# Kernel tuning notes

Hardware: AMD Instinct MI355X
Metric: run time of the kernel (lower is better)

## Reference

```python
import jax, jax.numpy as jnp
import numpy as np

# pywt 'db4' decomposition filters (8 taps)
DEC_LO = jnp.array([-0.010597401784997278, 0.032883011666982945, 0.030841381835986965,
                    -0.18703481171888114, -0.02798376941698385, 0.6308807679295904,
                    0.7148465705525415, 0.23037781330885523], dtype=jnp.float32)
DEC_HI = jnp.array([-0.23037781330885523, 0.7148465705525415, -0.6308807679295904,
                    -0.02798376941698385, 0.18703481171888114, 0.030841381835986965,
                    -0.032883011666982945, -0.010597401784997278], dtype=jnp.float32)
LEVELS = 3


def _dwt_step(sig, lo, hi):
    """One pywt dwt level, mode='symmetric'. sig: [M, S] -> (cA, cD) each [M, (S+F-1)//2]."""
    F = lo.shape[0]
    # symmetric extension by F-1 on each side; drop first sample so stride-2
    # correlation picks the odd-indexed valid-convolution outputs (pywt convention)
    ext = jnp.pad(sig, ((0, 0), (F - 1, F - 1)), mode='symmetric')[:, 1:]
    # true convolution = correlation with flipped filters
    kern = jnp.stack([lo[::-1], hi[::-1]])[:, None, :]          # [2, 1, F]
    y = jax.lax.conv_general_dilated(ext[:, None, :], kern, (2,), 'VALID')  # [M, 2, out]
    return y[:, 0], y[:, 1]


def _resize(c, T):
    """Match torch: truncate if longer than T, else F.interpolate linear align_corners=False."""
    S = c.shape[-1]
    if S == T:
        return c
    if S > T:
        return c[..., :T]
    pos = (jnp.arange(T, dtype=c.dtype) + 0.5) * (S / T) - 0.5
    pos = jnp.clip(pos, 0.0, S - 1)
    lo = jnp.floor(pos).astype(jnp.int32)
    hi = jnp.minimum(lo + 1, S - 1)
    w = pos - lo.astype(c.dtype)
    return c[..., lo] * (1.0 - w) + c[..., hi] * w


def setup_inputs() -> dict:
    key = jax.random.key(0)
    x = jax.random.normal(key, (16, 2048, 512, 1), dtype=jnp.float32)
    return {"x": x}


def reference(x):
    B, T, N, _ = x.shape
    sig = x[:, :, :, 0].transpose(0, 2, 1).reshape(B * N, T)  # [B*N, T]
    a = sig
    details = []
    for _ in range(LEVELS):
        a, d = _dwt_step(a, DEC_LO, DEC_HI)
        details.append(d)
    coeffs = [a] + details[::-1]  # pywt order: [cA_L, cD_L, ..., cD_1]
    out = jnp.stack([_resize(c, T) for c in coeffs], axis=-1)  # [B*N, T, L+1]
    return out.reshape(B, N, T, LEVELS + 1)
```

## Files before the change

### kernel.cpp

```cpp
#include <hip/hip_runtime.h>


#define TPB   256
#define ROWS  4
#define TLEN  2048
#define NCH   512
#define RSTRIDE 3080
#define CA3_OFF 0
#define CD3_OFF 520
#define CD2_OFF 1027
#define CD1_OFF 2048

typedef float f32x4 __attribute__((ext_vector_type(4)));

__constant__ float LO[8] = {-0.010597401784997278f,  0.032883011666982945f,  0.030841381835986965f,
                            -0.18703481171888114f,  -0.02798376941698385f,   0.6308807679295904f,
                             0.7148465705525415f,    0.23037781330885523f};
__constant__ float HI[8] = {-0.23037781330885523f,   0.7148465705525415f,   -0.6308807679295904f,
                            -0.02798376941698385f,   0.18703481171888114f,   0.030841381835986965f,
                            -0.032883011666982945f, -0.010597401784997278f};
__constant__ float RLO[8] = { 0.23037781330885523f,   0.7148465705525415f,   0.6308807679295904f,
                             -0.02798376941698385f,  -0.18703481171888114f,  0.030841381835986965f,
                              0.032883011666982945f, -0.010597401784997278f};
__constant__ float RHI[8] = {-0.010597401784997278f, -0.032883011666982945f, 0.030841381835986965f,
                              0.18703481171888114f,  -0.02798376941698385f,  -0.6308807679295904f,
                              0.7148465705525415f,   -0.23037781330885523f};

__device__ __forceinline__ int sym_idx(int e, int S) {
    int m = e - 6;
    m = (m < 0) ? (-1 - m) : m;
    m = (m >= S) ? (2 * S - 1 - m) : m;
    return m;
}

__device__ __forceinline__ void dwt_level_wave(float* rowp, int in_off, int S,
                                               int lo_off, int hi_off, int lane) {
    const int O    = (S + 7) >> 1;
    const int jmax = (S - 2) >> 1;
    for (int j = lane; j < O; j += 64) {
        float slo = 0.0f, shi = 0.0f;
        if (j >= 3 && j <= jmax) {
            const float* p = rowp + in_off + 2 * j - 6;
            float v[8];
            *(float2*)&v[0] = ((const float2*)p)[0];
            *(float2*)&v[2] = ((const float2*)p)[1];
            *(float2*)&v[4] = ((const float2*)p)[2];
            *(float2*)&v[6] = ((const float2*)p)[3];
            #pragma unroll
            for (int k = 0; k < 8; ++k) {
                slo = fmaf(RLO[k], v[k], slo);
                shi = fmaf(RHI[k], v[k], shi);
            }
        } else {
            const float* in = rowp + in_off;
            const int e0 = 2 * j + 7;
            #pragma unroll
            for (int k = 0; k < 8; ++k) {
                const float v = in[sym_idx(e0 - k, S)];
                slo = fmaf(LO[k], v, slo);
                shi = fmaf(HI[k], v, shi);
            }
        }
        rowp[lo_off + j] = slo;
        rowp[hi_off + j] = shi;
    }
}

__device__ __forceinline__ void lerp_coef(int S, int t, int& i0, int& i1, float& w) {
    const float scale = (float)S * (1.0f / 2048.0f);
    float p = ((float)t + 0.5f) * scale - 0.5f;
    p = fminf(fmaxf(p, 0.0f), (float)(S - 1));
    i0 = (int)p;
    i1 = min(i0 + 1, S - 1);
    w = p - (float)i0;
}

__device__ __forceinline__ float mix2(float a, float b, float w) {
    return a * (1.0f - w) + b * w;
}

__global__ __launch_bounds__(TPB)
void dwt_kernel(const float* __restrict__ x, float* __restrict__ out) {
    __shared__ float lds[ROWS * RSTRIDE];
    const int tid = threadIdx.x;

    const int nwg   = gridDim.x;
    const int chunk = nwg >> 3;
    const int p     = blockIdx.x;
    const int bid   = (p & 7) * chunk + (p >> 3);

    const int row0 = bid * ROWS;
    const int b    = row0 >> 9;
    const int n0   = row0 & 511;

    const float4* src = (const float4*)(x + (size_t)b * TLEN * NCH + n0);
    #pragma unroll
    for (int i = 0; i < TLEN / TPB; ++i) {
        const int t = tid + i * TPB;
        const float4 v = src[t * (NCH / 4)];
        lds[0 * RSTRIDE + t] = v.x;
        lds[1 * RSTRIDE + t] = v.y;
        lds[2 * RSTRIDE + t] = v.z;
        lds[3 * RSTRIDE + t] = v.w;
    }
    __syncthreads();

    const int wave = tid >> 6;
    const int lane = tid & 63;
    float* rowp = lds + wave * RSTRIDE;

    dwt_level_wave(rowp, 0, 2048, 0, CD1_OFF, lane);
    dwt_level_wave(rowp, 0, 1027, 0, CD2_OFF, lane);
    dwt_level_wave(rowp, 0,  517, 0, CD3_OFF, lane);

    f32x4* dst = (f32x4*)out + (size_t)(row0 + wave) * TLEN;
    #pragma unroll 4
    for (int i = 0; i < TLEN / 64; ++i) {
        const int t = lane + i * 64;
        int i0a, i1a; float wa; lerp_coef( 262, t, i0a, i1a, wa);
        int i0b, i1b; float wb; lerp_coef( 517, t, i0b, i1b, wb);
        int i0c, i1c; float wc; lerp_coef(1027, t, i0c, i1c, wc);
        f32x4 o;
        o.x = mix2(rowp[CA3_OFF + i0a], rowp[CA3_OFF + i1a], wa);
        o.y = mix2(rowp[CD3_OFF + i0a], rowp[CD3_OFF + i1a], wa);
        o.z = mix2(rowp[CD2_OFF + i0b], rowp[CD2_OFF + i1b], wb);
        o.w = mix2(rowp[CD1_OFF + i0c], rowp[CD1_OFF + i1c], wc);
        __builtin_nontemporal_store(o, &dst[t]);
    }
}

extern "C" void kernel_launch(void* const* d_in, const int* in_sizes, int n_in,
                              void* d_out, int out_size, void* d_ws, size_t ws_size,
                              hipStream_t stream) {
    const float* x = (const float*)d_in[0];
    float* out = (float*)d_out;
    const int n_rows = 16 * 512;
    dim3 grid(n_rows / ROWS), block(TPB);
    hipLaunchKernelGGL(dwt_kernel, grid, block, 0, stream, x, out);
}
```

Baseline: 66.08 us.

## Warp-specialize into a persistent double-buffered load/compute/store pipeline

Replaces the one-tile-per-block kernel with a persistent kernel of 256 blocks, each processing 8 row tiles. Within a block, two waves load input into a double-buffered LDS area, four waves run the three DWT levels, and four waves do the interpolation and stores, all synchronized by per-stage barriers. The DWT level function also moves the symmetric-boundary outputs into a separate pre-pass so the main loop has no branch. The aim is to overlap global loads, compute and stores across tiles, at the cost of about 130KB of LDS, one block per CU and fewer waves issuing memory traffic.

```diff
diff --git a/kernel.cpp b/kernel.cpp
--- a/kernel.cpp
+++ b/kernel.cpp
@@ -1,15 +1,19 @@
 #include <hip/hip_runtime.h>
 
 
-#define TPB   256
-#define ROWS  4
-#define TLEN  2048
-#define NCH   512
-#define RSTRIDE 3080
-#define CA3_OFF 0
-#define CD3_OFF 520
-#define CD2_OFF 1027
-#define CD1_OFF 2048
+#define TPB      640
+#define NT       8
+#define ROWS     4
+#define TLEN     2048
+#define NCH      512
+#define IBSTRIDE 2056
+#define CSTRIDE  2088
+#define CD1o 0
+#define CD2o 1032
+#define CD3o 1552
+#define CA3o 1816
+#define IB_FLOATS  (2 * ROWS * IBSTRIDE)
+#define LDS_BYTES  ((IB_FLOATS + 2 * ROWS * CSTRIDE) * 4)
 
 typedef float f32x4 __attribute__((ext_vector_type(4)));
 
@@ -26,6 +30,11 @@
                               0.18703481171888114f,  -0.02798376941698385f,  -0.6308807679295904f,
                               0.7148465705525415f,   -0.23037781330885523f};
 
+__device__ __forceinline__ void bar_lgkm() {
+    asm volatile("s_waitcnt lgkmcnt(0)" ::: "memory");
+    __builtin_amdgcn_s_barrier();
+}
+
 __device__ __forceinline__ int sym_idx(int e, int S) {
     int m = e - 6;
     m = (m < 0) ? (-1 - m) : m;
@@ -33,37 +42,41 @@
     return m;
 }
 
-__device__ __forceinline__ void dwt_level_wave(float* rowp, int in_off, int S,
-                                               int lo_off, int hi_off, int lane) {
+__device__ __forceinline__ void wave_level(const float* in, int S,
+                                           float* lo, float* hi, int lane) {
     const int O    = (S + 7) >> 1;
     const int jmax = (S - 2) >> 1;
-    for (int j = lane; j < O; j += 64) {
+    const int NB   = O - (jmax - 2);
+
+    float blo = 0.0f, bhi = 0.0f;
+    int bj = 0;
+    if (lane < NB) {
+        bj = (lane < 3) ? lane : (jmax + lane - 2);
+        const int e0 = 2 * bj + 7;
+        #pragma unroll
+        for (int k = 0; k < 8; ++k) {
+            const float v = in[sym_idx(e0 - k, S)];
+            blo = fmaf(LO[k], v, blo);
+            bhi = fmaf(HI[k], v, bhi);
+        }
+    }
+    for (int j = 3 + lane; j <= jmax; j += 64) {
+        const float* p = in + 2 * j - 6;
+        float v[8];
+        *(float2*)&v[0] = ((const float2*)p)[0];
+        *(float2*)&v[2] = ((const float2*)p)[1];
+        *(float2*)&v[4] = ((const float2*)p)[2];
+        *(float2*)&v[6] = ((const float2*)p)[3];
         float slo = 0.0f, shi = 0.0f;
-        if (j >= 3 && j <= jmax) {
-            const float* p = rowp + in_off + 2 * j - 6;
-            float v[8];
-            *(float2*)&v[0] = ((const float2*)p)[0];
-            *(float2*)&v[2] = ((const float2*)p)[1];
-            *(float2*)&v[4] = ((const float2*)p)[2];
-            *(float2*)&v[6] = ((const float2*)p)[3];
-            #pragma unroll
-            for (int k = 0; k < 8; ++k) {
-                slo = fmaf(RLO[k], v[k], slo);
-                shi = fmaf(RHI[k], v[k], shi);
-            }
-        } else {
-            const float* in = rowp + in_off;
-            const int e0 = 2 * j + 7;
-            #pragma unroll
-            for (int k = 0; k < 8; ++k) {
-                const float v = in[sym_idx(e0 - k, S)];
-                slo = fmaf(LO[k], v, slo);
-                shi = fmaf(HI[k], v, shi);
-            }
+        #pragma unroll
+        for (int k = 0; k < 8; ++k) {
+            slo = fmaf(RLO[k], v[k], slo);
+            shi = fmaf(RHI[k], v[k], shi);
         }
-        rowp[lo_off + j] = slo;
-        rowp[hi_off + j] = shi;
+        lo[j] = slo;
+        hi[j] = shi;
     }
+    if (lane < NB) { lo[bj] = blo; hi[bj] = bhi; }
 }
 
 __device__ __forceinline__ void lerp_coef(int S, int t, int& i0, int& i1, float& w) {
@@ -79,53 +92,89 @@
     return a * (1.0f - w) + b * w;
 }
 
+__device__ __forceinline__ int tile_row0(int p, int j) {
+    const int tile = (p & 7) * 256 + (p >> 3) + 32 * j;
+    return tile * ROWS;
+}
+
+__device__ __forceinline__ void load_tile(const float* __restrict__ x, int p, int j,
+                                          int lt, float4* pre) {
+    const int row0 = tile_row0(p, j);
+    const float4* s = (const float4*)(x + (size_t)(row0 >> 9) * TLEN * NCH + (row0 & 511));
+    #pragma unroll
+    for (int i = 0; i < 16; ++i) pre[i] = s[(lt + i * 128) * (NCH / 4)];
+}
+
+__device__ __forceinline__ void write_tile(float* ibase, int par, int lt, const float4* pre) {
+    float* b = ibase + par * ROWS * IBSTRIDE;
+    #pragma unroll
+    for (int i = 0; i < 16; ++i) {
+        const int t = lt + i * 128;
+        b[0 * IBSTRIDE + t] = pre[i].x;
+        b[1 * IBSTRIDE + t] = pre[i].y;
+        b[2 * IBSTRIDE + t] = pre[i].z;
+        b[3 * IBSTRIDE + t] = pre[i].w;
+    }
+}
+
 __global__ __launch_bounds__(TPB)
 void dwt_kernel(const float* __restrict__ x, float* __restrict__ out) {
-    __shared__ float lds[ROWS * RSTRIDE];
-    const int tid = threadIdx.x;
+    extern __shared__ float smem[];
+    float* ibase = smem;
+    float* cbase = smem + IB_FLOATS;
+    const int tid  = threadIdx.x;
+    const int wid  = tid >> 6;
+    const int lane = tid & 63;
+    const int p    = blockIdx.x;
 
-    const int nwg   = gridDim.x;
-    const int chunk = nwg >> 3;
-    const int p     = blockIdx.x;
-    const int bid   = (p & 7) * chunk + (p >> 3);
-
-    const int row0 = bid * ROWS;
-    const int b    = row0 >> 9;
-    const int n0   = row0 & 511;
-
-    const float4* src = (const float4*)(x + (size_t)b * TLEN * NCH + n0);
-    #pragma unroll
-    for (int i = 0; i < TLEN / TPB; ++i) {
-        const int t = tid + i * TPB;
-        const float4 v = src[t * (NCH / 4)];
-        lds[0 * RSTRIDE + t] = v.x;
-        lds[1 * RSTRIDE + t] = v.y;
-        lds[2 * RSTRIDE + t] = v.z;
-        lds[3 * RSTRIDE + t] = v.w;
-    }
-    __syncthreads();
-
-    const int wave = tid >> 6;
-    const int lane = tid & 63;
-    float* rowp = lds + wave * RSTRIDE;
-
-    dwt_level_wave(rowp, 0, 2048, 0, CD1_OFF, lane);
-    dwt_level_wave(rowp, 0, 1027, 0, CD2_OFF, lane);
-    dwt_level_wave(rowp, 0,  517, 0, CD3_OFF, lane);
-
-    f32x4* dst = (f32x4*)out + (size_t)(row0 + wave) * TLEN;
-    #pragma unroll 4
-    for (int i = 0; i < TLEN / 64; ++i) {
-        const int t = lane + i * 64;
-        int i0a, i1a; float wa; lerp_coef( 262, t, i0a, i1a, wa);
-        int i0b, i1b; float wb; lerp_coef( 517, t, i0b, i1b, wb);
-        int i0c, i1c; float wc; lerp_coef(1027, t, i0c, i1c, wc);
-        f32x4 o;
-        o.x = mix2(rowp[CA3_OFF + i0a], rowp[CA3_OFF + i1a], wa);
-        o.y = mix2(rowp[CD3_OFF + i0a], rowp[CD3_OFF + i1a], wa);
-        o.z = mix2(rowp[CD2_OFF + i0b], rowp[CD2_OFF + i1b], wb);
-        o.w = mix2(rowp[CD1_OFF + i0c], rowp[CD1_OFF + i1c], wc);
-        __builtin_nontemporal_store(o, &dst[t]);
+    if (wid >= 8) {
+        const int lt = tid - 512;
+        float4 pre[16];
+        load_tile(x, p, 0, lt, pre);
+        write_tile(ibase, 0, lt, pre);
+        bar_lgkm();
+        for (int j = 0; j <= NT; ++j) {
+            if (j + 1 < NT) {
+                load_tile(x, p, j + 1, lt, pre);
+                write_tile(ibase, (j + 1) & 1, lt, pre);
+            }
+            bar_lgkm();
+        }
+    } else if (wid < 4) {
+        bar_lgkm();
+        for (int j = 0; j <= NT; ++j) {
+            if (j < NT) {
+                float* a = ibase + ((j & 1) * ROWS + wid) * IBSTRIDE;
+                float* c = cbase + ((j & 1) * ROWS + wid) * CSTRIDE;
+                wave_level(a, 2048, a,        c + CD1o, lane);
+                wave_level(a, 1027, a,        c + CD2o, lane);
+                wave_level(a,  517, c + CA3o, c + CD3o, lane);
+            }
+            bar_lgkm();
+        }
+    } else {
+        const int r = wid - 4;
+        bar_lgkm();
+        for (int j = 0; j <= NT; ++j) {
+            if (j >= 1) {
+                const float* c = cbase + (((j - 1) & 1) * ROWS + r) * CSTRIDE;
+                const int row0 = tile_row0(p, j - 1);
+                f32x4* dst = (f32x4*)out + (size_t)(row0 + r) * TLEN;
+                for (int i = 0; i < TLEN / 64; ++i) {
+                    const int t = lane + (i << 6);
+                    int i0a, i1a; float wa; lerp_coef( 262, t, i0a, i1a, wa);
+                    int i0b, i1b; float wb; lerp_coef( 517, t, i0b, i1b, wb);
+                    int i0c, i1c; float wc; lerp_coef(1027, t, i0c, i1c, wc);
+                    f32x4 o;
+                    o.x = mix2(c[CA3o + i0a], c[CA3o + i1a], wa);
+                    o.y = mix2(c[CD3o + i0a], c[CD3o + i1a], wa);
+                    o.z = mix2(c[CD2o + i0b], c[CD2o + i1b], wb);
+                    o.w = mix2(c[CD1o + i0c], c[CD1o + i1c], wc);
+                    __builtin_nontemporal_store(o, &dst[t]);
+                }
+            }
+            bar_lgkm();
+        }
     }
 }
 
@@ -134,7 +183,7 @@
                               hipStream_t stream) {
     const float* x = (const float*)d_in[0];
     float* out = (float*)d_out;
-    const int n_rows = 16 * 512;
-    dim3 grid(n_rows / ROWS), block(TPB);
-    hipLaunchKernelGGL(dwt_kernel, grid, block, 0, stream, x, out);
+    hipFuncSetAttribute((const void*)dwt_kernel,
+                        hipFuncAttributeMaxDynamicSharedMemorySize, LDS_BYTES);
+    hipLaunchKernelGGL(dwt_kernel, dim3(256), dim3(TPB), LDS_BYTES, stream, x, out);
 }
```

After: 65.73 us. About the same (-0.5%).
